# Kernel tuning notes

Hardware: AMD Instinct MI355X
Metric: run time of the kernel (lower is better)

## Reference

```python
import jax, jax.numpy as jnp
import numpy as np

EMBED_DIM = 4096
NUM_HEADS = 64
RANK = 1
B, T = 64, 64  # T must equal NUM_HEADS for the mask broadcast (faithful to source)


def setup_inputs() -> dict:
    key = jax.random.key(0)
    k1, k2, k3, k4, k5 = jax.random.split(key, 5)
    C = EMBED_DIM
    s = 0.02
    return {
        "x": jax.random.normal(k1, (B, T, C), dtype=jnp.float32),
        "W_atten": jax.random.normal(k2, (3 * C, C), dtype=jnp.float32) * s,
        "b_atten": jax.random.normal(k3, (3 * C,), dtype=jnp.float32) * s,
        "W_proj": jax.random.normal(k4, (C, C), dtype=jnp.float32) * s,
        "b_proj": jax.random.normal(k5, (C,), dtype=jnp.float32) * s,
    }


def reference(x, W_atten, b_atten, W_proj, b_proj):
    Bx, Tx, C = x.shape
    H = NUM_HEADS
    hd = C // H
    r = RANK
    qkv = jnp.einsum("btc,oc->bto", x, W_atten) + b_atten  # (B,T,3C)
    q, k, v = jnp.split(qkv, 3, axis=2)
    # view (B,T,rank,H,hd) then transpose(1,2) -> (B,rank,T,H,hd)
    def reshp(t):
        return t.reshape(Bx, Tx, r, H, hd).transpose(0, 2, 1, 3, 4)
    q, k, v = reshp(q), reshp(k), reshp(v)
    scale = (1.0 / np.sqrt(hd)) * (r ** 0.5)
    # attention across heads at each timestep: (B,rank,T,H,H)
    att = jnp.einsum("brtqd,brtkd->brtqk", q, k) * scale
    # tril[:T,:T] broadcasts onto trailing (H,H) dims (requires T == H)
    tril = jnp.tril(jnp.ones((Tx, Tx), dtype=jnp.float32))
    att = jnp.where(tril == 0, -jnp.inf, att)
    att = jax.nn.softmax(att, axis=-1)
    y = jnp.einsum("brtqk,brtkd->brtqd", att, v)  # (B,rank,T,H,hd)
    y = y.transpose(0, 2, 1, 3, 4).reshape(Bx, Tx, C)
    return jnp.einsum("btc,oc->bto", y, W_proj) + b_proj
```

## Files before the change

### kernel.cpp

```cpp
#include <hip/hip_runtime.h>
#include <stdint.h>

#define M_TOK   4096
#define C_DIM   4096
#define N_QKV   12288

typedef __bf16 bf16x8 __attribute__((ext_vector_type(8)));
typedef float  f32x4  __attribute__((ext_vector_type(4)));
typedef unsigned short ushort8 __attribute__((ext_vector_type(8)));

__device__ __forceinline__ unsigned short f2bf(float f) {
  unsigned int u = __builtin_bit_cast(unsigned int, f);
  u = (u + 0x7FFFu + ((u >> 16) & 1u)) >> 16;
  return (unsigned short)u;
}
__device__ __forceinline__ float bf2f(unsigned short h) {
  unsigned int u = ((unsigned int)h) << 16;
  return __builtin_bit_cast(float, u);
}

__global__ __launch_bounds__(256) void cvt_f32_bf16(const float* __restrict__ in,
                                                    unsigned short* __restrict__ out,
                                                    int n16) {
  int idx = blockIdx.x * 256 + threadIdx.x;
  if (idx >= n16) return;
  const float4* p = (const float4*)in;
  float4 a = p[idx * 2], b = p[idx * 2 + 1];
  uint4 r;
  r.x = (unsigned)f2bf(a.x) | ((unsigned)f2bf(a.y) << 16);
  r.y = (unsigned)f2bf(a.z) | ((unsigned)f2bf(a.w) << 16);
  r.z = (unsigned)f2bf(b.x) | ((unsigned)f2bf(b.y) << 16);
  r.w = (unsigned)f2bf(b.z) | ((unsigned)f2bf(b.w) << 16);
  ((uint4*)out)[idx] = r;
}

#define GLLDS(gp, lp) \
  __builtin_amdgcn_global_load_lds((const __attribute__((address_space(1))) unsigned int*)(gp), \
                                   (__attribute__((address_space(3))) unsigned int*)(lp), 16, 0, 0)

template <int OUT_BF16>
__global__ __launch_bounds__(256, 3) void gemm_bt(const unsigned short* __restrict__ A,
                                                  const unsigned short* __restrict__ B,
                                                  const float* __restrict__ bias,
                                                  void* __restrict__ Cptr,
                                                  int M, int N, int K) {
  __shared__ __align__(16) unsigned short As[128 * 32];
  __shared__ __align__(16) unsigned short Bs[128 * 32];

  const int t  = threadIdx.x;
  const int bm = blockIdx.y;
  const int bn = blockIdx.x;
  const int w  = t >> 6;
  const int l  = t & 63;
  const int wm = (w >> 1) * 64;
  const int wn = (w & 1) * 64;
  const int lr = l & 15;
  const int lk = ((l >> 4) ^ ((lr >> 1) & 3)) * 8;

  const int srow = t >> 2;
  const int scol = ((t & 3) ^ ((t >> 3) & 3)) * 8;
  const unsigned short* ga0 = A + (size_t)(bm * 128 + srow) * K + scol;
  const unsigned short* ga1 = ga0 + (size_t)64 * K;
  const unsigned short* gb0 = B + (size_t)(bn * 128 + srow) * K + scol;
  const unsigned short* gb1 = gb0 + (size_t)64 * K;
  unsigned short* la0 = As + t * 8;
  unsigned short* la1 = As + t * 8 + 2048;
  unsigned short* lb0 = Bs + t * 8;
  unsigned short* lb1 = Bs + t * 8 + 2048;

  f32x4 acc[4][4] = {};

  for (int k0 = 0; k0 < K; k0 += 32) {
    GLLDS(ga0, la0);
    GLLDS(ga1, la1);
    GLLDS(gb0, lb0);
    GLLDS(gb1, lb1);
    ga0 += 32; ga1 += 32; gb0 += 32; gb1 += 32;
    __syncthreads();

    bf16x8 af[4], bf[4];
#pragma unroll
    for (int i = 0; i < 4; ++i)
      af[i] = *(const bf16x8*)(As + (wm + i * 16 + lr) * 32 + lk);
#pragma unroll
    for (int j = 0; j < 4; ++j)
      bf[j] = *(const bf16x8*)(Bs + (wn + j * 16 + lr) * 32 + lk);
#pragma unroll
    for (int i = 0; i < 4; ++i)
#pragma unroll
      for (int j = 0; j < 4; ++j)
        acc[i][j] = __builtin_amdgcn_mfma_f32_16x16x32_bf16(af[i], bf[j], acc[i][j], 0, 0, 0);
    __syncthreads();
  }

  const int row0 = bm * 128 + wm + (l >> 4) * 4;
  const int col0 = bn * 128 + wn + lr;
#pragma unroll
  for (int j = 0; j < 4; ++j) {
    const int col = col0 + j * 16;
    const float bv = bias[col];
#pragma unroll
    for (int i = 0; i < 4; ++i) {
      const int row = row0 + i * 16;
#pragma unroll
      for (int rg = 0; rg < 4; ++rg) {
        float v = acc[i][j][rg] + bv;
        if (OUT_BF16)
          ((unsigned short*)Cptr)[(size_t)(row + rg) * N + col] = f2bf(v);
        else
          ((float*)Cptr)[(size_t)(row + rg) * N + col] = v;
      }
    }
  }
}

#define AST 72

__global__ __launch_bounds__(64) void attn_mfma(const unsigned short* __restrict__ qkv,
                                                unsigned short* __restrict__ y) {
  __shared__ __align__(16) unsigned short Ks[64 * AST];
  __shared__ __align__(16) unsigned short Vs[64 * AST];
  const int l  = threadIdx.x;
  const int lr = l & 15;
  const int lq = l >> 4;
  const size_t base = (size_t)blockIdx.x * 12288;

  {
    const int jr = l >> 3;
    const int cc = (l & 7) * 8;
#pragma unroll
    for (int c = 0; c < 8; ++c) {
      const int j = c * 8 + jr;
      *(uint4*)(Ks + j * AST + cc) = *(const uint4*)(qkv + base + 4096 + (size_t)j * 64 + cc);
      *(uint4*)(Vs + j * AST + cc) = *(const uint4*)(qkv + base + 8192 + (size_t)j * 64 + cc);
    }
  }

  bf16x8 aq[4][2];
#pragma unroll
  for (int it = 0; it < 4; ++it)
#pragma unroll
    for (int kk = 0; kk < 2; ++kk)
      aq[it][kk] = *(const bf16x8*)(qkv + base + (size_t)(it * 16 + lr) * 64 + kk * 32 + lq * 8);

  __syncthreads();

  f32x4 acc[4][4] = {};
#pragma unroll
  for (int kk = 0; kk < 2; ++kk) {
    bf16x8 bk[4];
#pragma unroll
    for (int jt = 0; jt < 4; ++jt)
      bk[jt] = *(const bf16x8*)(Ks + (jt * 16 + lr) * AST + kk * 32 + lq * 8);
#pragma unroll
    for (int it = 0; it < 4; ++it)
#pragma unroll
      for (int jt = 0; jt < 4; ++jt)
        acc[it][jt] = __builtin_amdgcn_mfma_f32_16x16x32_bf16(aq[it][kk], bk[jt], acc[it][jt], 0, 0, 0);
  }

#pragma unroll
  for (int it = 0; it < 4; ++it) {
#pragma unroll
    for (int rg = 0; rg < 4; ++rg) {
      const int row = it * 16 + lq * 4 + rg;
      float mx = -1e30f;
#pragma unroll
      for (int jt = 0; jt < 4; ++jt) {
        const int col = jt * 16 + lr;
        float s = acc[it][jt][rg] * 0.125f;
        s = (col <= row) ? s : -1e30f;
        acc[it][jt][rg] = s;
        mx = fmaxf(mx, s);
      }
#pragma unroll
      for (int d = 1; d < 16; d <<= 1)
        mx = fmaxf(mx, __shfl_xor(mx, d));
      float sum = 0.f;
#pragma unroll
      for (int jt = 0; jt < 4; ++jt) {
        float e = __expf(acc[it][jt][rg] - mx);
        acc[it][jt][rg] = e;
        sum += e;
      }
#pragma unroll
      for (int d = 1; d < 16; d <<= 1)
        sum += __shfl_xor(sum, d);
      const float inv = 1.f / sum;
#pragma unroll
      for (int jt = 0; jt < 4; ++jt)
        acc[it][jt][rg] *= inv;
    }
  }

#pragma unroll
  for (int it = 0; it < 4; ++it)
#pragma unroll
    for (int rg = 0; rg < 4; ++rg) {
      const int row = it * 16 + lq * 4 + rg;
#pragma unroll
      for (int jt = 0; jt < 4; ++jt)
        Ks[row * AST + jt * 16 + lr] = f2bf(acc[it][jt][rg]);
    }
  __syncthreads();

  f32x4 out[4][4] = {};
#pragma unroll
  for (int kk = 0; kk < 2; ++kk) {
    bf16x8 ap[4];
#pragma unroll
    for (int it = 0; it < 4; ++it)
      ap[it] = *(const bf16x8*)(Ks + (it * 16 + lr) * AST + kk * 32 + lq * 8);
#pragma unroll
    for (int dt = 0; dt < 4; ++dt) {
      ushort8 vt;
#pragma unroll
      for (int jj = 0; jj < 8; ++jj)
        vt[jj] = Vs[(kk * 32 + lq * 8 + jj) * AST + dt * 16 + lr];
      const bf16x8 bv = __builtin_bit_cast(bf16x8, vt);
#pragma unroll
      for (int it = 0; it < 4; ++it)
        out[it][dt] = __builtin_amdgcn_mfma_f32_16x16x32_bf16(ap[it], bv, out[it][dt], 0, 0, 0);
    }
  }

  unsigned short* yrow = y + (size_t)blockIdx.x * 4096;
#pragma unroll
  for (int it = 0; it < 4; ++it)
#pragma unroll
    for (int rg = 0; rg < 4; ++rg) {
      const int i = it * 16 + lq * 4 + rg;
#pragma unroll
      for (int dt = 0; dt < 4; ++dt)
        yrow[i * 64 + dt * 16 + lr] = f2bf(out[it][dt][rg]);
    }
}

extern "C" void kernel_launch(void* const* d_in, const int* in_sizes, int n_in,
                              void* d_out, int out_size, void* d_ws, size_t ws_size,
                              hipStream_t stream) {
  const float* x  = (const float*)d_in[0];
  const float* Wa = (const float*)d_in[1];
  const float* ba = (const float*)d_in[2];
  const float* Wp = (const float*)d_in[3];
  const float* bp = (const float*)d_in[4];
  float* out = (float*)d_out;

  unsigned short* regA = (unsigned short*)d_ws;
  unsigned short* regB = regA + (size_t)16777216;
  unsigned short* regC = regB + (size_t)50331648;
  unsigned short* xb   = regA;
  unsigned short* Wab  = regB;
  unsigned short* qkvb = regC;
  unsigned short* Wpb  = regA;
  unsigned short* yb   = regB;

  cvt_f32_bf16<<<(16777216 / 8) / 256, 256, 0, stream>>>(x, xb, 16777216 / 8);
  cvt_f32_bf16<<<(50331648 / 8) / 256, 256, 0, stream>>>(Wa, Wab, 50331648 / 8);

  gemm_bt<1><<<dim3(N_QKV / 128, M_TOK / 128), 256, 0, stream>>>(
      xb, Wab, ba, (void*)qkvb, M_TOK, N_QKV, C_DIM);

  cvt_f32_bf16<<<(16777216 / 8) / 256, 256, 0, stream>>>(Wp, Wpb, 16777216 / 8);

  attn_mfma<<<M_TOK, 64, 0, stream>>>(qkvb, yb);

  gemm_bt<0><<<dim3(C_DIM / 128, M_TOK / 128), 256, 0, stream>>>(
      yb, Wpb, bp, (void*)out, M_TOK, C_DIM, C_DIM);
}
```

Baseline: 1.053 ms.

## Replace GEMM with 256x256 double-buffered pipelined kernel using 8 waves

Replaces the 128x128, single-buffered GEMM with a 256x256-tile kernel of 512 threads. It double-buffers 64-wide K slices in LDS, issues async global-to-LDS loads interleaved with MFMA phases, and uses s_setprio and explicit waitcnt/barriers. It also remaps block IDs with an XCD-aware swizzle and uses a new XOR swizzle for LDS bank conflicts. The goal is to hide memory latency and raise arithmetic intensity, at the cost of large LDS use (128KB per block) and hard-coded K and M sizes.

```diff
diff --git a/kernel.cpp b/kernel.cpp
--- a/kernel.cpp
+++ b/kernel.cpp
@@ -4,6 +4,8 @@
 #define M_TOK   4096
 #define C_DIM   4096
 #define N_QKV   12288
+#define KD      4096
+#define NT2     32
 
 typedef __bf16 bf16x8 __attribute__((ext_vector_type(8)));
 typedef float  f32x4  __attribute__((ext_vector_type(4)));
@@ -38,80 +40,156 @@
   __builtin_amdgcn_global_load_lds((const __attribute__((address_space(1))) unsigned int*)(gp), \
                                    (__attribute__((address_space(3))) unsigned int*)(lp), 16, 0, 0)
 
+
+#define STAGE_A(buf, hf, tau) do {                                         \
+    const unsigned short* g_ = Ag + (size_t)((hf) * 64) * KD + (tau) * 64; \
+    unsigned short* d_ = As + (buf) * 16384 + (hf) * 8192 + t * 8;         \
+    GLLDS(g_, d_);                                                         \
+    GLLDS(g_ + (size_t)128 * KD, d_ + 4096);                               \
+  } while (0)
+
+#define STAGE_B(buf, nhf, tau) do {                                         \
+    const unsigned short* g_ = Bg + (size_t)((nhf) * 32) * KD + (tau) * 64; \
+    unsigned short* d_ = Bs + (buf) * 16384 + (nhf) * 8192 + t * 8;         \
+    GLLDS(g_, d_);                                                          \
+    GLLDS(g_ + (size_t)128 * KD, d_ + 4096);                                \
+  } while (0)
+
+#define LDA_(buf, mh) do {                                                        \
+    const unsigned short* pa_ = As + (buf) * 16384 + (mh) * 8192 + wm * 4096 + lr * 64; \
+    _Pragma("unroll") for (int mt_ = 0; mt_ < 4; ++mt_) {                         \
+      afk[0][mt_] = *(const bf16x8*)(pa_ + mt_ * 1024 + ck0);                     \
+      afk[1][mt_] = *(const bf16x8*)(pa_ + mt_ * 1024 + ck1);                     \
+    }                                                                             \
+  } while (0)
+
+#define LDB_(buf, nhf, dst) do {                                                  \
+    const unsigned short* pb_ = Bs + (buf) * 16384 + (nhf) * 8192 + wn * 2048 + lr * 64; \
+    _Pragma("unroll") for (int nt_ = 0; nt_ < 2; ++nt_) {                         \
+      dst[0][nt_] = *(const bf16x8*)(pb_ + nt_ * 1024 + ck0);                     \
+      dst[1][nt_] = *(const bf16x8*)(pb_ + nt_ * 1024 + ck1);                     \
+    }                                                                             \
+  } while (0)
+
+#define QUAD_(mh, nhf, bsrc) do {                                                 \
+    _Pragma("unroll") for (int kk_ = 0; kk_ < 2; ++kk_)                           \
+    _Pragma("unroll") for (int mt_ = 0; mt_ < 4; ++mt_)                           \
+    _Pragma("unroll") for (int nt_ = 0; nt_ < 2; ++nt_)                           \
+      acc[mh][nhf][mt_][nt_] = __builtin_amdgcn_mfma_f32_16x16x32_bf16(           \
+          afk[kk_][mt_], bsrc[kk_][nt_], acc[mh][nhf][mt_][nt_], 0, 0, 0);        \
+  } while (0)
+
+#define PH_MID() do {                                      \
+    asm volatile("" ::: "memory");                         \
+    __builtin_amdgcn_s_barrier();                          \
+    asm volatile("s_waitcnt lgkmcnt(0)" ::: "memory");     \
+    __builtin_amdgcn_s_setprio(1);                         \
+  } while (0)
+
+#define PH_END() do {                                      \
+    __builtin_amdgcn_s_setprio(0);                         \
+    asm volatile("" ::: "memory");                         \
+    __builtin_amdgcn_s_barrier();                          \
+    asm volatile("" ::: "memory");                         \
+  } while (0)
+
+#define PH_END_VM() do {                                   \
+    __builtin_amdgcn_s_setprio(0);                         \
+    asm volatile("s_waitcnt vmcnt(6)" ::: "memory");       \
+    __builtin_amdgcn_s_barrier();                          \
+    asm volatile("" ::: "memory");                         \
+  } while (0)
+
 template <int OUT_BF16>
-__global__ __launch_bounds__(256, 3) void gemm_bt(const unsigned short* __restrict__ A,
+__global__ __launch_bounds__(512, 2) void gemm256(const unsigned short* __restrict__ A,
                                                   const unsigned short* __restrict__ B,
                                                   const float* __restrict__ bias,
                                                   void* __restrict__ Cptr,
-                                                  int M, int N, int K) {
-  __shared__ __align__(16) unsigned short As[128 * 32];
-  __shared__ __align__(16) unsigned short Bs[128 * 32];
-
-  const int t  = threadIdx.x;
-  const int bm = blockIdx.y;
-  const int bn = blockIdx.x;
-  const int w  = t >> 6;
-  const int l  = t & 63;
-  const int wm = (w >> 1) * 64;
-  const int wn = (w & 1) * 64;
-  const int lr = l & 15;
-  const int lk = ((l >> 4) ^ ((lr >> 1) & 3)) * 8;
-
-  const int srow = t >> 2;
-  const int scol = ((t & 3) ^ ((t >> 3) & 3)) * 8;
-  const unsigned short* ga0 = A + (size_t)(bm * 128 + srow) * K + scol;
-  const unsigned short* ga1 = ga0 + (size_t)64 * K;
-  const unsigned short* gb0 = B + (size_t)(bn * 128 + srow) * K + scol;
-  const unsigned short* gb1 = gb0 + (size_t)64 * K;
-  unsigned short* la0 = As + t * 8;
-  unsigned short* la1 = As + t * 8 + 2048;
-  unsigned short* lb0 = Bs + t * 8;
-  unsigned short* lb1 = Bs + t * 8 + 2048;
-
-  f32x4 acc[4][4] = {};
-
-  for (int k0 = 0; k0 < K; k0 += 32) {
-    GLLDS(ga0, la0);
-    GLLDS(ga1, la1);
-    GLLDS(gb0, lb0);
-    GLLDS(gb1, lb1);
-    ga0 += 32; ga1 += 32; gb0 += 32; gb1 += 32;
-    __syncthreads();
-
-    bf16x8 af[4], bf[4];
-#pragma unroll
-    for (int i = 0; i < 4; ++i)
-      af[i] = *(const bf16x8*)(As + (wm + i * 16 + lr) * 32 + lk);
-#pragma unroll
-    for (int j = 0; j < 4; ++j)
-      bf[j] = *(const bf16x8*)(Bs + (wn + j * 16 + lr) * 32 + lk);
-#pragma unroll
-    for (int i = 0; i < 4; ++i)
-#pragma unroll
-      for (int j = 0; j < 4; ++j)
-        acc[i][j] = __builtin_amdgcn_mfma_f32_16x16x32_bf16(af[i], bf[j], acc[i][j], 0, 0, 0);
-    __syncthreads();
-  }
-
-  const int row0 = bm * 128 + wm + (l >> 4) * 4;
-  const int col0 = bn * 128 + wn + lr;
-#pragma unroll
-  for (int j = 0; j < 4; ++j) {
-    const int col = col0 + j * 16;
-    const float bv = bias[col];
-#pragma unroll
-    for (int i = 0; i < 4; ++i) {
-      const int row = row0 + i * 16;
-#pragma unroll
-      for (int rg = 0; rg < 4; ++rg) {
-        float v = acc[i][j][rg] + bv;
-        if (OUT_BF16)
-          ((unsigned short*)Cptr)[(size_t)(row + rg) * N + col] = f2bf(v);
-        else
-          ((float*)Cptr)[(size_t)(row + rg) * N + col] = v;
-      }
-    }
-  }
+                                                  int N) {
+  __shared__ __align__(16) unsigned short As[32768];
+  __shared__ __align__(16) unsigned short Bs[32768];
+
+  const int t   = threadIdx.x;
+  const int nwg = gridDim.x;
+  const int bid = blockIdx.x;
+  const int wg  = (bid & 7) * (nwg >> 3) + (bid >> 3);
+  const int bm  = wg & 15;
+  const int bn  = wg >> 4;
+
+  const int w  = t >> 6, l = t & 63;
+  const int wm = w >> 2, wn = w & 3;
+  const int lr = l & 15, lq = l >> 4;
+  const int ck0 = (lq ^ (lr & 7)) * 8;
+  const int ck1 = ck0 ^ 32;
+
+  const int r8  = t >> 3;
+  const int kcs = ((t & 7) ^ (r8 & 7)) * 8;
+  const unsigned short* Ag = A + (size_t)(bm * 256 + r8) * KD + kcs;
+  const unsigned short* Bg = B + (size_t)(bn * 256 + ((t >> 8) << 6) + (r8 & 31)) * KD + kcs;
+
+  f32x4 acc[2][2][4][2] = {};
+  bf16x8 afk[2][4], bA[2][2], bB[2][2];
+
+  STAGE_A(0, 0, 0); STAGE_B(0, 0, 0); STAGE_B(0, 1, 0); STAGE_A(0, 1, 0);
+  STAGE_A(1, 0, 1); STAGE_B(1, 0, 1); STAGE_B(1, 1, 1);
+  asm volatile("s_waitcnt vmcnt(6)" ::: "memory");
+  __builtin_amdgcn_s_barrier();
+  asm volatile("" ::: "memory");
+
+#pragma unroll 1
+  for (int i = 0; i < NT2; ++i) {
+    const int t1 = 2 * i + 1;
+    const int t2 = (2 * i + 2 < 64) ? 2 * i + 2 : 63;
+    const int t3 = (2 * i + 3 < 64) ? 2 * i + 3 : 63;
+    LDA_(0, 0); LDB_(0, 0, bA);
+    STAGE_A(1, 1, t1);
+    PH_MID(); QUAD_(0, 0, bA); PH_END();
+    LDB_(0, 1, bB);
+    STAGE_A(0, 0, t2);
+    PH_MID(); QUAD_(0, 1, bB); PH_END();
+    LDA_(0, 1);
+    STAGE_B(0, 0, t2);
+    PH_MID(); QUAD_(1, 0, bA); PH_END();
+    STAGE_B(0, 1, t2);
+    PH_MID(); QUAD_(1, 1, bB); PH_END_VM();
+    LDA_(1, 0); LDB_(1, 0, bA);
+    STAGE_A(0, 1, t2);
+    PH_MID(); QUAD_(0, 0, bA); PH_END();
+    LDB_(1, 1, bB);
+    STAGE_A(1, 0, t3);
+    PH_MID(); QUAD_(0, 1, bB); PH_END();
+    LDA_(1, 1);
+    STAGE_B(1, 0, t3);
+    PH_MID(); QUAD_(1, 0, bA); PH_END();
+    STAGE_B(1, 1, t3);
+    PH_MID(); QUAD_(1, 1, bB); PH_END_VM();
+  }
+
+  asm volatile("s_waitcnt vmcnt(0)" ::: "memory");
+
+  const int row0 = bm * 256 + wm * 128 + lq * 4;
+  const int col0 = bn * 256 + wn * 64 + lr;
+#pragma unroll
+  for (int nhf = 0; nhf < 2; ++nhf)
+#pragma unroll
+    for (int nt = 0; nt < 2; ++nt) {
+      const int col = col0 + nhf * 32 + nt * 16;
+      const float bv = bias[col];
+#pragma unroll
+      for (int mh = 0; mh < 2; ++mh)
+#pragma unroll
+        for (int mt = 0; mt < 4; ++mt) {
+          const int row = row0 + mh * 64 + mt * 16;
+#pragma unroll
+          for (int rg = 0; rg < 4; ++rg) {
+            float v = acc[mh][nhf][mt][nt][rg] + bv;
+            if (OUT_BF16)
+              ((unsigned short*)Cptr)[(size_t)(row + rg) * N + col] = f2bf(v);
+            else
+              ((float*)Cptr)[(size_t)(row + rg) * N + col] = v;
+          }
+        }
+    }
 }
 
 #define AST 72
@@ -258,13 +336,13 @@
   cvt_f32_bf16<<<(16777216 / 8) / 256, 256, 0, stream>>>(x, xb, 16777216 / 8);
   cvt_f32_bf16<<<(50331648 / 8) / 256, 256, 0, stream>>>(Wa, Wab, 50331648 / 8);
 
-  gemm_bt<1><<<dim3(N_QKV / 128, M_TOK / 128), 256, 0, stream>>>(
-      xb, Wab, ba, (void*)qkvb, M_TOK, N_QKV, C_DIM);
+  gemm256<1><<<dim3((M_TOK / 256) * (N_QKV / 256)), dim3(512), 0, stream>>>(
+      xb, Wab, ba, (void*)qkvb, N_QKV);
 
   cvt_f32_bf16<<<(16777216 / 8) / 256, 256, 0, stream>>>(Wp, Wpb, 16777216 / 8);
 
   attn_mfma<<<M_TOK, 64, 0, stream>>>(qkvb, yb);
 
-  gemm_bt<0><<<dim3(C_DIM / 128, M_TOK / 128), 256, 0, stream>>>(
-      yb, Wpb, bp, (void*)out, M_TOK, C_DIM, C_DIM);
-}
+  gemm256<0><<<dim3((M_TOK / 256) * (C_DIM / 256)), dim3(512), 0, stream>>>(
+      yb, Wpb, bp, (void*)out, C_DIM);
+}
```

Result: faster. 961.2 us (-8.7%).
